# Kernel optimization log

Measured on AMD Instinct MI355X. Metric: run time of the kernel, lower is better.

## Reference

```python
import jax, jax.numpy as jnp
import numpy as np

N = 50000          # number of nodes
NNZ = 800000       # edges per relation (avg degree 16)
R = 3              # edge_features / number of relations
D_IN = 128
D_OUT = 128
EPS = 1e-6


def setup_inputs() -> dict:
    key = jax.random.key(0)
    ks = jax.random.split(key, 8)
    return {
        "input": jax.random.normal(ks[0], (N, D_IN), dtype=jnp.float32),
        "adj_rows": jax.random.randint(ks[1], (R, NNZ), 0, N, dtype=jnp.int64) if jax.config.jax_enable_x64 else jax.random.randint(ks[1], (R, NNZ), 0, N).astype(jnp.int32),
        "adj_cols": jax.random.randint(ks[2], (R, NNZ), 0, N, dtype=jnp.int64) if jax.config.jax_enable_x64 else jax.random.randint(ks[2], (R, NNZ), 0, N).astype(jnp.int32),
        "adj_vals": jax.random.uniform(ks[3], (R, NNZ), dtype=jnp.float32),
        "weight": jax.random.normal(ks[4], (D_IN * R, D_OUT), dtype=jnp.float32) * (1.0 / np.sqrt(D_OUT)),
        "share_weight": jax.random.normal(ks[5], (D_IN, D_OUT), dtype=jnp.float32) * (1.0 / np.sqrt(D_OUT)),
        "bias": jax.random.normal(ks[6], (D_OUT,), dtype=jnp.float32) * (1.0 / np.sqrt(D_OUT)),
        "ln_gamma": jnp.ones((D_IN,), dtype=jnp.float32),
        "ln_beta": jnp.zeros((D_IN,), dtype=jnp.float32),
    }


def _spmm(rows, cols, vals, x, n_nodes):
    # (sparse A) @ x via gather + segment-sum: out[r] = sum_{e: rows[e]=r} vals[e]*x[cols[e]]
    msgs = vals[:, None] * x[cols]            # [nnz, d]
    return jax.ops.segment_sum(msgs, rows, num_segments=n_nodes)


def _layernorm(x, gamma, beta):
    mu = jnp.mean(x, axis=-1, keepdims=True)
    var = jnp.var(x, axis=-1, keepdims=True)
    return (x - mu) * jax.lax.rsqrt(var + EPS) * gamma + beta


def reference(input, adj_rows, adj_cols, adj_vals, weight, share_weight, bias, ln_gamma, ln_beta):
    n = input.shape[0]
    # loop over the small fixed relation set to keep peak memory low
    support_list = [
        _spmm(adj_rows[r], adj_cols[r], adj_vals[r], input, n) for r in range(adj_rows.shape[0])
    ]
    support = jnp.concatenate(support_list, axis=1)   # [N, R*d_in]
    support_sum = support_list[0]
    for s in support_list[1:]:
        support_sum = support_sum + s
    support_norm = _layernorm(support_sum, ln_gamma, ln_beta)
    out = (support @ weight + support_norm @ share_weight) * 0.5
    return out + bias
```

## Files before the change

kernel.cpp:

```cpp
#include <hip/hip_runtime.h>
#include <hip/hip_fp16.h>

constexpr int NN  = 50000;
constexpr int NNZ = 800000;
constexpr int RR  = 3;
constexpr int D   = 128;
constexpr int RN  = RR * NN;
constexpr int NE  = RR * NNZ;
constexpr int KK  = 512;
constexpr int MPAD = 50048;
constexpr int PART = 256;
constexpr int PSZ  = (RN + PART - 1) / PART;
constexpr int CAP  = 10240;
constexpr int EPB  = 2048;
constexpr float EPS = 1e-6f;

constexpr int NB_SPLIT = (NE + EPB - 1) / EPB;
constexpr int NB_XH    = (NN * 64 + 255) / 256;
constexpr int NB_WT    = 256;

using bf16x8 = __attribute__((ext_vector_type(8))) __bf16;
using f32x4  = __attribute__((ext_vector_type(4))) float;

__device__ __forceinline__ unsigned pack_bf2(float a, float b) {
  unsigned ua = __float_as_uint(a); ua = (ua + (0x7FFFu + ((ua >> 16) & 1))) >> 16;
  unsigned ub = __float_as_uint(b); ub = (ub + (0x7FFFu + ((ub >> 16) & 1))) >> 16;
  return ua | (ub << 16);
}
__device__ __forceinline__ unsigned bf16_lo(float a) {
  unsigned ua = __float_as_uint(a);
  return (ua + (0x7FFFu + ((ua >> 16) & 1))) >> 16;
}

__device__ __forceinline__ void gload16(const void* g, void* l) {
  __builtin_amdgcn_global_load_lds(
      (const __attribute__((address_space(1))) unsigned int*)g,
      (__attribute__((address_space(3))) unsigned int*)l, 16, 0, 0);
}

__device__ __forceinline__ float val16(unsigned u) {
  return __half2float(__ushort_as_half((unsigned short)(u & 0xFFFFu)));
}

#define ACC2(accA, accB, word, vv) {                                   \
    __half2 _h = __builtin_bit_cast(__half2, (word));                  \
    accA = __builtin_fmaf(__half2float(_h.x), (vv), accA);             \
    accB = __builtin_fmaf(__half2float(_h.y), (vv), accB); }

__global__ __launch_bounds__(256) void prep(
    const int*   __restrict__ rows,
    const int*   __restrict__ cols,
    const float* __restrict__ vals,
    const float* __restrict__ x,
    const float* __restrict__ w,
    const float* __restrict__ shw,
    int*   __restrict__ pcur,
    uint2* __restrict__ pedges,
    unsigned* __restrict__ xh,
    unsigned short* __restrict__ WT) {
  __shared__ uint2 sbuf[EPB];
  __shared__ int lcur[PART];
  __shared__ int lstart[PART];
  __shared__ int lbase[PART];
  __shared__ int sdata[256];
  int blk = blockIdx.x;
  int t = threadIdx.x;

  if (blk >= NB_SPLIT) {
    int b2 = blk - NB_SPLIT;
    if (b2 < NB_XH) {
      int i = b2 * 256 + t;
      float2 v = ((const float2*)x)[i];
      xh[i] = __builtin_bit_cast(unsigned, __floats2half2_rn(v.x, v.y));
    } else {
      int idx = (b2 - NB_XH) * 256 + t;
      int k   = idx >> 7;
      int col = idx & 127;
      float v = (k < 384) ? w[k * 128 + col] : shw[(k - 384) * 128 + col];
      WT[col * 512 + k] = (unsigned short)bf16_lo(v);
    }
    return;
  }

  lcur[t] = 0;
  __syncthreads();

  int e0 = blk * EPB;
  int nvalid = min(EPB, NE - e0);
  constexpr int EPT = EPB / 256;
  int ebk[EPT]; unsigned epay[EPT];
  #pragma unroll
  for (int j = 0; j < EPT; j++) {
    int e = e0 + j * 256 + t;
    if (e < NE) {
      int r = (e >= 2 * NNZ) ? 2 : (e >= NNZ ? 1 : 0);
      int b = r * NN + rows[e];
      ebk[j] = b;
      epay[j] = ((unsigned)cols[e] << 16) |
                (unsigned)__half_as_ushort(__float2half_rn(vals[e]));
      atomicAdd(&lcur[b / PSZ], 1);
    } else {
      ebk[j] = -1;
    }
  }
  __syncthreads();

  int cnt = lcur[t];
  sdata[t] = cnt;
  __syncthreads();
  #pragma unroll
  for (int step = 1; step < 256; step <<= 1) {
    int v = (t >= step) ? sdata[t - step] : 0;
    __syncthreads();
    sdata[t] += v;
    __syncthreads();
  }
  int excl = sdata[t] - cnt;
  lstart[t] = excl;
  lbase[t] = atomicAdd(&pcur[t], cnt);
  __syncthreads();
  lcur[t] = excl;
  __syncthreads();

  #pragma unroll
  for (int j = 0; j < EPT; j++) {
    if (ebk[j] >= 0) {
      int pos = atomicAdd(&lcur[ebk[j] / PSZ], 1);
      sbuf[pos] = make_uint2((unsigned)ebk[j], epay[j]);
    }
  }
  __syncthreads();

  for (int i = t; i < nvalid; i += 256) {
    uint2 ed = sbuf[i];
    int p = (int)(ed.x / PSZ);
    pedges[(size_t)p * CAP + lbase[p] + (i - lstart[p])] = ed;
  }
}

__global__ __launch_bounds__(512) void sort_part(
    const uint2* __restrict__ pedges,
    const int*   __restrict__ pcur,
    int* __restrict__ off,
    unsigned* __restrict__ epack) {
  __shared__ int sc[PSZ];
  __shared__ int sdata[512];
  int p = blockIdx.x;
  int t = threadIdx.x;
  int bb = p * PSZ;
  int nbuck = min(PSZ, RN - bb);
  int n = pcur[p];
  const uint2* src = pedges + (size_t)p * CAP;

  sdata[t] = (t < p && t < PART) ? pcur[t] : 0;
  __syncthreads();
  #pragma unroll
  for (int step = 256; step >= 1; step >>= 1) {
    if (t < step) sdata[t] += sdata[t + step];
    __syncthreads();
  }
  int gbase = sdata[0];
  __syncthreads();
  if (p == 0 && t == 0) off[RN] = NE;

  for (int i = t; i < nbuck; i += 512) sc[i] = 0;
  __syncthreads();
  for (int i = t; i < n; i += 512)
    atomicAdd(&sc[src[i].x - bb], 1);
  __syncthreads();

  constexpr int PER = (PSZ + 511) / 512;
  int lo = t * PER, hi = min(lo + PER, nbuck);
  int s = 0;
  for (int i = lo; i < hi; i++) s += sc[i];
  sdata[t] = s;
  __syncthreads();
  #pragma unroll
  for (int step = 1; step < 512; step <<= 1) {
    int v = (t >= step) ? sdata[t - step] : 0;
    __syncthreads();
    sdata[t] += v;
    __syncthreads();
  }
  int run = gbase + sdata[t] - s;
  for (int i = lo; i < hi; i++) {
    int c = sc[i];
    sc[i] = run;
    off[bb + i] = run;
    run += c;
  }
  __syncthreads();

  for (int i = t; i < n; i += 512) {
    uint2 ed = src[i];
    int pos = atomicAdd(&sc[ed.x - bb], 1);
    epack[pos] = ed.y;
  }
}

__global__ __launch_bounds__(256) void gather_ln(
    const unsigned* __restrict__ xh,
    const unsigned* __restrict__ epack,
    const int*      __restrict__ off,
    const float* __restrict__ gamma,
    const float* __restrict__ beta,
    unsigned* __restrict__ Au) {
  int node = blockIdx.x * 4 + (threadIdx.x >> 6);
  if (node >= NN) return;
  int lane = threadIdx.x & 63;
  int g  = lane >> 4;
  int q  = lane & 15;
  const unsigned* xq = xh + q * 4;

  float l0=0,l1=0,l2=0,l3=0,l4=0,l5=0,l6=0,l7=0;

  #pragma unroll
  for (int r = 0; r < RR; r++) {
    int b = r * NN + node;
    int s = off[b], e2 = off[b + 1];
    float a0=0,a1=0,a2=0,a3=0,a4=0,a5=0,a6=0,a7=0;

    for (int i0 = s; i0 < e2; i0 += 64) {
      int navail = min(64, e2 - i0);
      unsigned ep = (lane < navail) ? epack[i0 + lane] : 0u;
      int c0 = 0;
      for (; c0 + 16 <= navail; c0 += 16) {
        unsigned ua = __shfl(ep, c0 + g);
        unsigned ub = __shfl(ep, c0 + 4 + g);
        unsigned uc = __shfl(ep, c0 + 8 + g);
        unsigned ud = __shfl(ep, c0 + 12 + g);
        uint4 ga = *(const uint4*)(xq + (size_t)(ua >> 16) * 64);
        uint4 gb = *(const uint4*)(xq + (size_t)(ub >> 16) * 64);
        uint4 gc = *(const uint4*)(xq + (size_t)(uc >> 16) * 64);
        uint4 gd = *(const uint4*)(xq + (size_t)(ud >> 16) * 64);
        float va = val16(ua), vb = val16(ub), vc = val16(uc), vd = val16(ud);
        ACC2(a0,a1,ga.x,va) ACC2(a2,a3,ga.y,va) ACC2(a4,a5,ga.z,va) ACC2(a6,a7,ga.w,va)
        ACC2(a0,a1,gb.x,vb) ACC2(a2,a3,gb.y,vb) ACC2(a4,a5,gb.z,vb) ACC2(a6,a7,gb.w,vb)
        ACC2(a0,a1,gc.x,vc) ACC2(a2,a3,gc.y,vc) ACC2(a4,a5,gc.z,vc) ACC2(a6,a7,gc.w,vc)
        ACC2(a0,a1,gd.x,vd) ACC2(a2,a3,gd.y,vd) ACC2(a4,a5,gd.z,vd) ACC2(a6,a7,gd.w,vd)
      }
      for (; c0 + 4 <= navail; c0 += 4) {
        unsigned u = __shfl(ep, c0 + g);
        uint4 gg = *(const uint4*)(xq + (size_t)(u >> 16) * 64);
        float v = val16(u);
        ACC2(a0,a1,gg.x,v) ACC2(a2,a3,gg.y,v) ACC2(a4,a5,gg.z,v) ACC2(a6,a7,gg.w,v)
      }
      if (c0 < navail) {
        int eidx = c0 + g;
        unsigned u = __shfl(ep, min(eidx, navail - 1));
        float v = (eidx < navail) ? val16(u) : 0.0f;
        uint4 gg = *(const uint4*)(xq + (size_t)(u >> 16) * 64);
        ACC2(a0,a1,gg.x,v) ACC2(a2,a3,gg.y,v) ACC2(a4,a5,gg.z,v) ACC2(a6,a7,gg.w,v)
      }
    }
    #define REDG(x) x += __shfl_xor(x, 16); x += __shfl_xor(x, 32);
    REDG(a0) REDG(a1) REDG(a2) REDG(a3) REDG(a4) REDG(a5) REDG(a6) REDG(a7)
    #undef REDG
    if (g == 0) {
      uint4 w;
      w.x = pack_bf2(a0, a1); w.y = pack_bf2(a2, a3);
      w.z = pack_bf2(a4, a5); w.w = pack_bf2(a6, a7);
      *(uint4*)(Au + (size_t)node * 256 + r * 64 + q * 4) = w;
    }
    l0 += a0; l1 += a1; l2 += a2; l3 += a3;
    l4 += a4; l5 += a5; l6 += a6; l7 += a7;
  }

  float sum = l0+l1+l2+l3+l4+l5+l6+l7;
  float sq  = l0*l0+l1*l1+l2*l2+l3*l3+l4*l4+l5*l5+l6*l6+l7*l7;
  #pragma unroll
  for (int m = 1; m <= 8; m <<= 1) {
    sum += __shfl_xor(sum, m);
    sq  += __shfl_xor(sq,  m);
  }
  float mean = sum * (1.0f / D);
  float var  = sq * (1.0f / D) - mean * mean;
  float rstd = rsqrtf(var + EPS);
  float4 gm0 = *(const float4*)&gamma[8 * q];
  float4 gm1 = *(const float4*)&gamma[8 * q + 4];
  float4 bt0 = *(const float4*)&beta[8 * q];
  float4 bt1 = *(const float4*)&beta[8 * q + 4];
  float o0 = (l0 - mean) * rstd * gm0.x + bt0.x;
  float o1 = (l1 - mean) * rstd * gm0.y + bt0.y;
  float o2 = (l2 - mean) * rstd * gm0.z + bt0.z;
  float o3 = (l3 - mean) * rstd * gm0.w + bt0.w;
  float o4 = (l4 - mean) * rstd * gm1.x + bt1.x;
  float o5 = (l5 - mean) * rstd * gm1.y + bt1.y;
  float o6 = (l6 - mean) * rstd * gm1.z + bt1.z;
  float o7 = (l7 - mean) * rstd * gm1.w + bt1.w;
  if (g == 0) {
    uint4 w;
    w.x = pack_bf2(o0, o1); w.y = pack_bf2(o2, o3);
    w.z = pack_bf2(o4, o5); w.w = pack_bf2(o6, o7);
    *(uint4*)(Au + (size_t)node * 256 + 192 + q * 4) = w;
  }
}

__global__ __launch_bounds__(512) void gemm_mfma(
    const char* __restrict__ Ab,
    const char* __restrict__ Bb,
    const float* __restrict__ bias,
    float* __restrict__ out) {
  __shared__ __align__(16) char smem[32768];
  char* As = smem;
  char* Bs = smem + 16384;

  int tid  = threadIdx.x;
  int wid  = tid >> 6;
  int lane = tid & 63;
  int wr   = wid >> 1;
  int wc   = wid & 1;
  int row0 = blockIdx.x * 128;

  f32x4 zero = {0.f, 0.f, 0.f, 0.f};
  f32x4 acc[2][4];
  #pragma unroll
  for (int i = 0; i < 2; i++)
    #pragma unroll
    for (int j = 0; j < 4; j++) acc[i][j] = zero;

  for (int kc = 0; kc < 8; kc++) {
    #pragma unroll
    for (int i = 0; i < 2; i++) {
      int c = i * 512 + tid;
      int r = c >> 3, s = c & 7;
      int ss = s ^ (r & 7);
      const void* src = Ab + (size_t)(row0 + r) * 1024 + kc * 128 + ss * 16;
      void* dst = As + i * 8192 + wid * 1024;
      gload16(src, dst);
    }
    #pragma unroll
    for (int i = 0; i < 2; i++) {
      int c = i * 512 + tid;
      int r = c >> 3, s = c & 7;
      int ss = s ^ (r & 7);
      const void* src = Bb + (size_t)r * 1024 + kc * 128 + ss * 16;
      void* dst = Bs + i * 8192 + wid * 1024;
      gload16(src, dst);
    }
    __syncthreads();

    #pragma unroll
    for (int ks = 0; ks < 2; ks++) {
      bf16x8 afrag[2], bfrag[4];
      int sg = ks * 4 + (lane >> 4);
      #pragma unroll
      for (int rb = 0; rb < 2; rb++) {
        int r = wr * 32 + rb * 16 + (lane & 15);
        afrag[rb] = *(const bf16x8*)(As + r * 128 + (sg ^ (r & 7)) * 16);
      }
      #pragma unroll
      for (int cb = 0; cb < 4; cb++) {
        int col = wc * 64 + cb * 16 + (lane & 15);
        bfrag[cb] = *(const bf16x8*)(Bs + col * 128 + (sg ^ (col & 7)) * 16);
      }
      #pragma unroll
      for (int rb = 0; rb < 2; rb++)
        #pragma unroll
        for (int cb = 0; cb < 4; cb++)
          acc[rb][cb] = __builtin_amdgcn_mfma_f32_16x16x32_bf16(
              afrag[rb], bfrag[cb], acc[rb][cb], 0, 0, 0);
    }
    __syncthreads();
  }

  #pragma unroll
  for (int rb = 0; rb < 2; rb++) {
    #pragma unroll
    for (int cb = 0; cb < 4; cb++) {
      int col = wc * 64 + cb * 16 + (lane & 15);
      float bv = bias[col];
      #pragma unroll
      for (int r = 0; r < 4; r++) {
        int grow = row0 + wr * 32 + rb * 16 + (lane >> 4) * 4 + r;
        if (grow < NN) out[(size_t)grow * 128 + col] = 0.5f * acc[rb][cb][r] + bv;
      }
    }
  }
}

extern "C" void kernel_launch(void* const* d_in, const int* in_sizes, int n_in,
                              void* d_out, int out_size, void* d_ws, size_t ws_size,
                              hipStream_t stream) {
  const float* input  = (const float*)d_in[0];
  const int*   arows  = (const int*)  d_in[1];
  const int*   acols  = (const int*)  d_in[2];
  const float* avals  = (const float*)d_in[3];
  const float* weight = (const float*)d_in[4];
  const float* shw    = (const float*)d_in[5];
  const float* bias   = (const float*)d_in[6];
  const float* gamma  = (const float*)d_in[7];
  const float* beta   = (const float*)d_in[8];
  float* out = (float*)d_out;

  char* ws = (char*)d_ws;
  char*  Abf   = ws;                         ws += (size_t)MPAD * KK * 2;
  unsigned short* WT = (unsigned short*)ws;  ws += (size_t)128 * KK * 2;
  unsigned* xh  = (unsigned*)ws;             ws += (size_t)NN * 64 * 4;
  uint2* pedges = (uint2*)ws;                ws += (size_t)PART * CAP * sizeof(uint2);
  unsigned* epack = (unsigned*)ws;           ws += (size_t)NE * 4;
  int*   off   = (int*)ws;                   ws += ((size_t)RN + 4) * sizeof(int);
  int*   pcur  = (int*)ws;                   ws += (size_t)PART * sizeof(int);

  hipMemsetAsync(pcur, 0, (size_t)PART * sizeof(int), stream);
  prep      <<<NB_SPLIT + NB_XH + NB_WT, 256, 0, stream>>>(
                arows, acols, avals, input, weight, shw, pcur, pedges, xh, WT);
  sort_part <<<PART, 512, 0, stream>>>(pedges, pcur, off, epack);
  gather_ln <<<(NN + 3) / 4, 256, 0, stream>>>(xh, epack, off, gamma, beta,
                                               (unsigned*)Abf);
  gemm_mfma <<<MPAD / 128, 512, 0, stream>>>(Abf, (const char*)WT, bias, out);
}
```

Measured before the change: 168.5 us.

## Fuse gather/layernorm with MFMA GEMM via LDS-resident activation tile

Merges the gather+layernorm kernel and the separate GEMM kernel into one. Each block of four waves aggregates 32 nodes into a swizzled bf16 tile in LDS, then runs MFMA against the weight matrix read directly from global memory. This removes the 50 MB bf16 intermediate write and read and one kernel launch. In exchange, each wave now processes 8 nodes serially instead of one node per wave, and weight fragments are re-read from global/L2 by every block without LDS staging, which can cut gather parallelism and add memory traffic.

```diff
diff --git a/kernel.cpp b/kernel.cpp
--- a/kernel.cpp
+++ b/kernel.cpp
@@ -7,12 +7,11 @@
 constexpr int D   = 128;
 constexpr int RN  = RR * NN;
 constexpr int NE  = RR * NNZ;
-constexpr int KK  = 512;
-constexpr int MPAD = 50048;
 constexpr int PART = 256;
 constexpr int PSZ  = (RN + PART - 1) / PART;
 constexpr int CAP  = 10240;
 constexpr int EPB  = 2048;
+constexpr int NPB  = 32;
 constexpr float EPS = 1e-6f;
 
 constexpr int NB_SPLIT = (NE + EPB - 1) / EPB;
@@ -30,12 +29,6 @@
 __device__ __forceinline__ unsigned bf16_lo(float a) {
   unsigned ua = __float_as_uint(a);
   return (ua + (0x7FFFu + ((ua >> 16) & 1))) >> 16;
-}
-
-__device__ __forceinline__ void gload16(const void* g, void* l) {
-  __builtin_amdgcn_global_load_lds(
-      (const __attribute__((address_space(1))) unsigned int*)g,
-      (__attribute__((address_space(3))) unsigned int*)l, 16, 0, 0);
 }
 
 __device__ __forceinline__ float val16(unsigned u) {
@@ -198,182 +191,157 @@
   }
 }
 
-__global__ __launch_bounds__(256) void gather_ln(
+__global__ __launch_bounds__(256) void gather_gemm(
     const unsigned* __restrict__ xh,
     const unsigned* __restrict__ epack,
     const int*      __restrict__ off,
     const float* __restrict__ gamma,
     const float* __restrict__ beta,
-    unsigned* __restrict__ Au) {
-  int node = blockIdx.x * 4 + (threadIdx.x >> 6);
-  if (node >= NN) return;
-  int lane = threadIdx.x & 63;
+    const char*  __restrict__ WTb,
+    const float* __restrict__ bias,
+    float* __restrict__ out) {
+  __shared__ __align__(16) char A_lds[NPB * 1024];
+  int n0   = blockIdx.x * NPB;
+  int t    = threadIdx.x;
+  int wv   = t >> 6;
+  int lane = t & 63;
   int g  = lane >> 4;
   int q  = lane & 15;
   const unsigned* xq = xh + q * 4;
 
-  float l0=0,l1=0,l2=0,l3=0,l4=0,l5=0,l6=0,l7=0;
-
-  #pragma unroll
-  for (int r = 0; r < RR; r++) {
-    int b = r * NN + node;
-    int s = off[b], e2 = off[b + 1];
-    float a0=0,a1=0,a2=0,a3=0,a4=0,a5=0,a6=0,a7=0;
-
-    for (int i0 = s; i0 < e2; i0 += 64) {
-      int navail = min(64, e2 - i0);
-      unsigned ep = (lane < navail) ? epack[i0 + lane] : 0u;
-      int c0 = 0;
-      for (; c0 + 16 <= navail; c0 += 16) {
-        unsigned ua = __shfl(ep, c0 + g);
-        unsigned ub = __shfl(ep, c0 + 4 + g);
-        unsigned uc = __shfl(ep, c0 + 8 + g);
-        unsigned ud = __shfl(ep, c0 + 12 + g);
-        uint4 ga = *(const uint4*)(xq + (size_t)(ua >> 16) * 64);
-        uint4 gb = *(const uint4*)(xq + (size_t)(ub >> 16) * 64);
-        uint4 gc = *(const uint4*)(xq + (size_t)(uc >> 16) * 64);
-        uint4 gd = *(const uint4*)(xq + (size_t)(ud >> 16) * 64);
-        float va = val16(ua), vb = val16(ub), vc = val16(uc), vd = val16(ud);
-        ACC2(a0,a1,ga.x,va) ACC2(a2,a3,ga.y,va) ACC2(a4,a5,ga.z,va) ACC2(a6,a7,ga.w,va)
-        ACC2(a0,a1,gb.x,vb) ACC2(a2,a3,gb.y,vb) ACC2(a4,a5,gb.z,vb) ACC2(a6,a7,gb.w,vb)
-        ACC2(a0,a1,gc.x,vc) ACC2(a2,a3,gc.y,vc) ACC2(a4,a5,gc.z,vc) ACC2(a6,a7,gc.w,vc)
-        ACC2(a0,a1,gd.x,vd) ACC2(a2,a3,gd.y,vd) ACC2(a4,a5,gd.z,vd) ACC2(a6,a7,gd.w,vd)
+  for (int i = 0; i < 8; i++) {
+    int row  = wv * 8 + i;
+    int node = n0 + row;
+    if (node >= NN) {
+      uint4 z = make_uint4(0, 0, 0, 0);
+      *(uint4*)(A_lds + row * 1024 + lane * 16) = z;
+      continue;
+    }
+    float l0=0,l1=0,l2=0,l3=0,l4=0,l5=0,l6=0,l7=0;
+
+    #pragma unroll
+    for (int r = 0; r < RR; r++) {
+      int b = r * NN + node;
+      int s = off[b], e2 = off[b + 1];
+      float a0=0,a1=0,a2=0,a3=0,a4=0,a5=0,a6=0,a7=0;
+
+      for (int i0 = s; i0 < e2; i0 += 64) {
+        int navail = min(64, e2 - i0);
+        unsigned ep = (lane < navail) ? epack[i0 + lane] : 0u;
+        int c0 = 0;
+        for (; c0 + 16 <= navail; c0 += 16) {
+          unsigned ua = __shfl(ep, c0 + g);
+          unsigned ub = __shfl(ep, c0 + 4 + g);
+          unsigned uc = __shfl(ep, c0 + 8 + g);
+          unsigned ud = __shfl(ep, c0 + 12 + g);
+          uint4 ga = *(const uint4*)(xq + (size_t)(ua >> 16) * 64);
+          uint4 gb = *(const uint4*)(xq + (size_t)(ub >> 16) * 64);
+          uint4 gc = *(const uint4*)(xq + (size_t)(uc >> 16) * 64);
+          uint4 gd = *(const uint4*)(xq + (size_t)(ud >> 16) * 64);
+          float va = val16(ua), vb = val16(ub), vc = val16(uc), vd = val16(ud);
+          ACC2(a0,a1,ga.x,va) ACC2(a2,a3,ga.y,va) ACC2(a4,a5,ga.z,va) ACC2(a6,a7,ga.w,va)
+          ACC2(a0,a1,gb.x,vb) ACC2(a2,a3,gb.y,vb) ACC2(a4,a5,gb.z,vb) ACC2(a6,a7,gb.w,vb)
+          ACC2(a0,a1,gc.x,vc) ACC2(a2,a3,gc.y,vc) ACC2(a4,a5,gc.z,vc) ACC2(a6,a7,gc.w,vc)
+          ACC2(a0,a1,gd.x,vd) ACC2(a2,a3,gd.y,vd) ACC2(a4,a5,gd.z,vd) ACC2(a6,a7,gd.w,vd)
+        }
+        for (; c0 + 4 <= navail; c0 += 4) {
+          unsigned u = __shfl(ep, c0 + g);
+          uint4 gg = *(const uint4*)(xq + (size_t)(u >> 16) * 64);
+          float v = val16(u);
+          ACC2(a0,a1,gg.x,v) ACC2(a2,a3,gg.y,v) ACC2(a4,a5,gg.z,v) ACC2(a6,a7,gg.w,v)
+        }
+        if (c0 < navail) {
+          int eidx = c0 + g;
+          unsigned u = __shfl(ep, min(eidx, navail - 1));
+          float v = (eidx < navail) ? val16(u) : 0.0f;
+          uint4 gg = *(const uint4*)(xq + (size_t)(u >> 16) * 64);
+          ACC2(a0,a1,gg.x,v) ACC2(a2,a3,gg.y,v) ACC2(a4,a5,gg.z,v) ACC2(a6,a7,gg.w,v)
+        }
       }
-      for (; c0 + 4 <= navail; c0 += 4) {
-        unsigned u = __shfl(ep, c0 + g);
-        uint4 gg = *(const uint4*)(xq + (size_t)(u >> 16) * 64);
-        float v = val16(u);
-        ACC2(a0,a1,gg.x,v) ACC2(a2,a3,gg.y,v) ACC2(a4,a5,gg.z,v) ACC2(a6,a7,gg.w,v)
+      #define REDG(x) x += __shfl_xor(x, 16); x += __shfl_xor(x, 32);
+      REDG(a0) REDG(a1) REDG(a2) REDG(a3) REDG(a4) REDG(a5) REDG(a6) REDG(a7)
+      #undef REDG
+      if (g == 0) {
+        uint4 w;
+        w.x = pack_bf2(a0, a1); w.y = pack_bf2(a2, a3);
+        w.z = pack_bf2(a4, a5); w.w = pack_bf2(a6, a7);
+        int slot = (r * 16 + q) ^ (row & 7);
+        *(uint4*)(A_lds + row * 1024 + slot * 16) = w;
       }
-      if (c0 < navail) {
-        int eidx = c0 + g;
-        unsigned u = __shfl(ep, min(eidx, navail - 1));
-        float v = (eidx < navail) ? val16(u) : 0.0f;
-        uint4 gg = *(const uint4*)(xq + (size_t)(u >> 16) * 64);
-        ACC2(a0,a1,gg.x,v) ACC2(a2,a3,gg.y,v) ACC2(a4,a5,gg.z,v) ACC2(a6,a7,gg.w,v)
-      }
-    }
-    #define REDG(x) x += __shfl_xor(x, 16); x += __shfl_xor(x, 32);
-    REDG(a0) REDG(a1) REDG(a2) REDG(a3) REDG(a4) REDG(a5) REDG(a6) REDG(a7)
-    #undef REDG
+      l0 += a0; l1 += a1; l2 += a2; l3 += a3;
+      l4 += a4; l5 += a5; l6 += a6; l7 += a7;
+    }
+
+    float sum = l0+l1+l2+l3+l4+l5+l6+l7;
+    float sq  = l0*l0+l1*l1+l2*l2+l3*l3+l4*l4+l5*l5+l6*l6+l7*l7;
+    #pragma unroll
+    for (int m = 1; m <= 8; m <<= 1) {
+      sum += __shfl_xor(sum, m);
+      sq  += __shfl_xor(sq,  m);
+    }
+    float mean = sum * (1.0f / D);
+    float var  = sq * (1.0f / D) - mean * mean;
+    float rstd = rsqrtf(var + EPS);
+    float4 gm0 = *(const float4*)&gamma[8 * q];
+    float4 gm1 = *(const float4*)&gamma[8 * q + 4];
+    float4 bt0 = *(const float4*)&beta[8 * q];
+    float4 bt1 = *(const float4*)&beta[8 * q + 4];
+    float o0 = (l0 - mean) * rstd * gm0.x + bt0.x;
+    float o1 = (l1 - mean) * rstd * gm0.y + bt0.y;
+    float o2 = (l2 - mean) * rstd * gm0.z + bt0.z;
+    float o3 = (l3 - mean) * rstd * gm0.w + bt0.w;
+    float o4 = (l4 - mean) * rstd * gm1.x + bt1.x;
+    float o5 = (l5 - mean) * rstd * gm1.y + bt1.y;
+    float o6 = (l6 - mean) * rstd * gm1.z + bt1.z;
+    float o7 = (l7 - mean) * rstd * gm1.w + bt1.w;
     if (g == 0) {
       uint4 w;
-      w.x = pack_bf2(a0, a1); w.y = pack_bf2(a2, a3);
-      w.z = pack_bf2(a4, a5); w.w = pack_bf2(a6, a7);
-      *(uint4*)(Au + (size_t)node * 256 + r * 64 + q * 4) = w;
-    }
-    l0 += a0; l1 += a1; l2 += a2; l3 += a3;
-    l4 += a4; l5 += a5; l6 += a6; l7 += a7;
-  }
-
-  float sum = l0+l1+l2+l3+l4+l5+l6+l7;
-  float sq  = l0*l0+l1*l1+l2*l2+l3*l3+l4*l4+l5*l5+l6*l6+l7*l7;
-  #pragma unroll
-  for (int m = 1; m <= 8; m <<= 1) {
-    sum += __shfl_xor(sum, m);
-    sq  += __shfl_xor(sq,  m);
-  }
-  float mean = sum * (1.0f / D);
-  float var  = sq * (1.0f / D) - mean * mean;
-  float rstd = rsqrtf(var + EPS);
-  float4 gm0 = *(const float4*)&gamma[8 * q];
-  float4 gm1 = *(const float4*)&gamma[8 * q + 4];
-  float4 bt0 = *(const float4*)&beta[8 * q];
-  float4 bt1 = *(const float4*)&beta[8 * q + 4];
-  float o0 = (l0 - mean) * rstd * gm0.x + bt0.x;
-  float o1 = (l1 - mean) * rstd * gm0.y + bt0.y;
-  float o2 = (l2 - mean) * rstd * gm0.z + bt0.z;
-  float o3 = (l3 - mean) * rstd * gm0.w + bt0.w;
-  float o4 = (l4 - mean) * rstd * gm1.x + bt1.x;
-  float o5 = (l5 - mean) * rstd * gm1.y + bt1.y;
-  float o6 = (l6 - mean) * rstd * gm1.z + bt1.z;
-  float o7 = (l7 - mean) * rstd * gm1.w + bt1.w;
-  if (g == 0) {
-    uint4 w;
-    w.x = pack_bf2(o0, o1); w.y = pack_bf2(o2, o3);
-    w.z = pack_bf2(o4, o5); w.w = pack_bf2(o6, o7);
-    *(uint4*)(Au + (size_t)node * 256 + 192 + q * 4) = w;
-  }
-}
-
-__global__ __launch_bounds__(512) void gemm_mfma(
-    const char* __restrict__ Ab,
-    const char* __restrict__ Bb,
-    const float* __restrict__ bias,
-    float* __restrict__ out) {
-  __shared__ __align__(16) char smem[32768];
-  char* As = smem;
-  char* Bs = smem + 16384;
-
-  int tid  = threadIdx.x;
-  int wid  = tid >> 6;
-  int lane = tid & 63;
-  int wr   = wid >> 1;
-  int wc   = wid & 1;
-  int row0 = blockIdx.x * 128;
+      w.x = pack_bf2(o0, o1); w.y = pack_bf2(o2, o3);
+      w.z = pack_bf2(o4, o5); w.w = pack_bf2(o6, o7);
+      int slot = (48 + q) ^ (row & 7);
+      *(uint4*)(A_lds + row * 1024 + slot * 16) = w;
+    }
+  }
+  __syncthreads();
 
   f32x4 zero = {0.f, 0.f, 0.f, 0.f};
-  f32x4 acc[2][4];
-  #pragma unroll
-  for (int i = 0; i < 2; i++)
-    #pragma unroll
-    for (int j = 0; j < 4; j++) acc[i][j] = zero;
-
-  for (int kc = 0; kc < 8; kc++) {
-    #pragma unroll
-    for (int i = 0; i < 2; i++) {
-      int c = i * 512 + tid;
-      int r = c >> 3, s = c & 7;
-      int ss = s ^ (r & 7);
-      const void* src = Ab + (size_t)(row0 + r) * 1024 + kc * 128 + ss * 16;
-      void* dst = As + i * 8192 + wid * 1024;
-      gload16(src, dst);
-    }
-    #pragma unroll
-    for (int i = 0; i < 2; i++) {
-      int c = i * 512 + tid;
-      int r = c >> 3, s = c & 7;
-      int ss = s ^ (r & 7);
-      const void* src = Bb + (size_t)r * 1024 + kc * 128 + ss * 16;
-      void* dst = Bs + i * 8192 + wid * 1024;
-      gload16(src, dst);
-    }
-    __syncthreads();
-
-    #pragma unroll
-    for (int ks = 0; ks < 2; ks++) {
-      bf16x8 afrag[2], bfrag[4];
-      int sg = ks * 4 + (lane >> 4);
+  f32x4 acc[2][2];
+  acc[0][0] = zero; acc[0][1] = zero; acc[1][0] = zero; acc[1][1] = zero;
+  int ks = lane >> 4;
+  int lr = lane & 15;
+  #pragma unroll
+  for (int kk = 0; kk < 16; kk++) {
+    bf16x8 af[2], bfr[2];
+    #pragma unroll
+    for (int m = 0; m < 2; m++) {
+      int row = m * 16 + lr;
+      int slot = (kk * 4 + ks) ^ (row & 7);
+      af[m] = *(const bf16x8*)(A_lds + row * 1024 + slot * 16);
+    }
+    #pragma unroll
+    for (int n = 0; n < 2; n++) {
+      int col = (wv * 2 + n) * 16 + lr;
+      bfr[n] = *(const bf16x8*)(WTb + (size_t)col * 1024 + kk * 64 + ks * 16);
+    }
+    #pragma unroll
+    for (int m = 0; m < 2; m++)
       #pragma unroll
-      for (int rb = 0; rb < 2; rb++) {
-        int r = wr * 32 + rb * 16 + (lane & 15);
-        afrag[rb] = *(const bf16x8*)(As + r * 128 + (sg ^ (r & 7)) * 16);
-      }
-      #pragma unroll
-      for (int cb = 0; cb < 4; cb++) {
-        int col = wc * 64 + cb * 16 + (lane & 15);
-        bfrag[cb] = *(const bf16x8*)(Bs + col * 128 + (sg ^ (col & 7)) * 16);
-      }
-      #pragma unroll
-      for (int rb = 0; rb < 2; rb++)
-        #pragma unroll
-        for (int cb = 0; cb < 4; cb++)
-          acc[rb][cb] = __builtin_amdgcn_mfma_f32_16x16x32_bf16(
-              afrag[rb], bfrag[cb], acc[rb][cb], 0, 0, 0);
-    }
-    __syncthreads();
-  }
-
-  #pragma unroll
-  for (int rb = 0; rb < 2; rb++) {
-    #pragma unroll
-    for (int cb = 0; cb < 4; cb++) {
-      int col = wc * 64 + cb * 16 + (lane & 15);
-      float bv = bias[col];
+      for (int n = 0; n < 2; n++)
+        acc[m][n] = __builtin_amdgcn_mfma_f32_16x16x32_bf16(
+            af[m], bfr[n], acc[m][n], 0, 0, 0);
+  }
+
+  #pragma unroll
+  for (int n = 0; n < 2; n++) {
+    int col = (wv * 2 + n) * 16 + lr;
+    float bv = bias[col];
+    #pragma unroll
+    for (int m = 0; m < 2; m++) {
       #pragma unroll
       for (int r = 0; r < 4; r++) {
-        int grow = row0 + wr * 32 + rb * 16 + (lane >> 4) * 4 + r;
-        if (grow < NN) out[(size_t)grow * 128 + col] = 0.5f * acc[rb][cb][r] + bv;
+        int row = m * 16 + (lane >> 4) * 4 + r;
+        int node = n0 + row;
+        if (node < NN) out[(size_t)node * 128 + col] = 0.5f * acc[m][n][r] + bv;
       }
     }
   }
@@ -394,8 +362,7 @@
   float* out = (float*)d_out;
 
   char* ws = (char*)d_ws;
-  char*  Abf   = ws;                         ws += (size_t)MPAD * KK * 2;
-  unsigned short* WT = (unsigned short*)ws;  ws += (size_t)128 * KK * 2;
+  unsigned short* WT = (unsigned short*)ws;  ws += (size_t)128 * 512 * 2;
   unsigned* xh  = (unsigned*)ws;             ws += (size_t)NN * 64 * 4;
   uint2* pedges = (uint2*)ws;                ws += (size_t)PART * CAP * sizeof(uint2);
   unsigned* epack = (unsigned*)ws;           ws += (size_t)NE * 4;
@@ -403,10 +370,9 @@
   int*   pcur  = (int*)ws;                   ws += (size_t)PART * sizeof(int);
 
   hipMemsetAsync(pcur, 0, (size_t)PART * sizeof(int), stream);
-  prep      <<<NB_SPLIT + NB_XH + NB_WT, 256, 0, stream>>>(
-                arows, acols, avals, input, weight, shw, pcur, pedges, xh, WT);
-  sort_part <<<PART, 512, 0, stream>>>(pedges, pcur, off, epack);
-  gather_ln <<<(NN + 3) / 4, 256, 0, stream>>>(xh, epack, off, gamma, beta,
-                                               (unsigned*)Abf);
-  gemm_mfma <<<MPAD / 128, 512, 0, stream>>>(Abf, (const char*)WT, bias, out);
-}
+  prep        <<<NB_SPLIT + NB_XH + NB_WT, 256, 0, stream>>>(
+                  arows, acols, avals, input, weight, shw, pcur, pedges, xh, WT);
+  sort_part   <<<PART, 512, 0, stream>>>(pedges, pcur, off, epack);
+  gather_gemm <<<(NN + NPB - 1) / NPB, 256, 0, stream>>>(
+                  xh, epack, off, gamma, beta, (const char*)WT, bias, out);
+}
```

New measurement: 216.5 us. 28.5% more time.
